# Performance work log

Hardware: AMD Instinct MI355X
Metric: run time of the kernel (lower is better)

## Reference

```python
import jax, jax.numpy as jnp
import numpy as np
import math

B, C, H, W, S = 8, 512, 64, 64, 4


def setup_inputs() -> dict:
    key = jax.random.key(0)
    ks = jax.random.split(key, 7)
    s = 1.0 / math.sqrt(C)  # ~ torch Linear init scale
    x = jax.random.normal(ks[0], (B, C, H, W), jnp.float32)
    Wq = jax.random.uniform(ks[1], (C, C), jnp.float32, -s, s)
    bq = jax.random.uniform(ks[2], (C,), jnp.float32, -s, s)
    Wk = jax.random.uniform(ks[3], (C, C), jnp.float32, -s, s)
    bk = jax.random.uniform(ks[4], (C,), jnp.float32, -s, s)
    Wv = jax.random.uniform(ks[5], (C, C), jnp.float32, -s, s)
    bv = jax.random.uniform(ks[6], (C,), jnp.float32, -s, s)
    return {"x": x, "Wq": Wq, "bq": bq, "Wk": Wk, "bk": bk, "Wv": Wv, "bv": bv}


def reference(x, Wq, bq, Wk, bk, Wv, bv):
    # x: (B, C, H, W). Faithful to the torch module's output, but expressed
    # in the algebraically-equivalent efficient form: the repeat_interleaved
    # attention matrix A is block-constant, so out = repeat(A_m @ Vsum).
    b, c, h, w = x.shape
    nb = (h // S) * (w // S)  # number of SxS spatial blocks
    hw = h * w
    ss = S * S

    # Block means in unfold order (bh, bw): (B, nb, C)
    x_avg = x.reshape(b, c, h // S, S, w // S, S).mean(axis=(3, 5))
    x_avg = x_avg.reshape(b, c, nb).transpose(0, 2, 1)

    Q = x_avg @ Wq.T + bq  # (B, nb, C)
    K = x_avg @ Wk.T + bk  # (B, nb, C)
    A = jax.nn.softmax(jnp.einsum('bnc,bmc->bnm', Q, K) / jnp.sqrt(jnp.float32(c)), axis=-1)

    # V over flat row-major pixels: (B, HW, C)
    x_flat = x.reshape(b, c, hw).transpose(0, 2, 1)
    V = x_flat @ Wv.T + bv

    # repeat_interleave on dim=2 means column group j of A sums V rows
    # [j*ss, (j+1)*ss) in FLAT pixel order (not spatial blocks) - faithful.
    Vsum = V.reshape(b, hw // ss, ss, c).sum(axis=2)  # (B, nb, C)
    out_small = jnp.einsum('bnm,bmc->bnc', A, Vsum)   # (B, nb, C)
    # repeat_interleave on dim=1: each block row broadcast to ss flat pixels
    out_flat = jnp.repeat(out_small, ss, axis=1)      # (B, HW, C)
    return out_flat.transpose(0, 2, 1).reshape(b, c, h, w)
```

## Files before the change

kernel.cpp:

```cpp
#include <hip/hip_runtime.h>

typedef __attribute__((ext_vector_type(8))) short short8;
typedef __attribute__((ext_vector_type(4))) float f32x4;

__device__ __forceinline__ unsigned short f2bf(float f) {
    union { float f; unsigned int i; } v; v.f = f;
    unsigned int x = v.i;
    return (unsigned short)((x + 0x7FFFu + ((x >> 16) & 1u)) >> 16);
}
__device__ __forceinline__ f32x4 mfma16(short8 a, short8 b, f32x4 c) {
    return __builtin_amdgcn_mfma_f32_16x16x32_bf16(a, b, c, 0, 0, 0);
}

__global__ void prep_kernel(const float* __restrict__ x,
                            const float* __restrict__ Wq,
                            const float* __restrict__ Wk,
                            const float* __restrict__ Wv,
                            unsigned short* __restrict__ xavg,
                            unsigned short* __restrict__ xsum,
                            unsigned short* __restrict__ Wb)
{
    const int blk = blockIdx.x;
    const int t = threadIdx.x;
    if (blk >= 4096) {
        const int f = (blk - 4096) * 512 + t;
        const int m = f >> 16;
        const int o = f & 65535;
        const float4* s4 = (const float4*)((m == 0) ? Wq : (m == 1) ? Wk : Wv);
        float4 a = s4[o];
        float4 b = s4[o + 256];
        ushort4* d4 = (ushort4*)(Wb + (size_t)m * 262144);
        d4[o]       = make_ushort4(f2bf(a.x), f2bf(a.y), f2bf(a.z), f2bf(a.w));
        d4[o + 256] = make_ushort4(f2bf(b.x), f2bf(b.y), f2bf(b.z), f2bf(b.w));
        return;
    }
    const int b = blk >> 9;
    const int c = blk & 511;

    const float4* x4 = (const float4*)(x + (size_t)blk * 4096);
    float4 f0 = x4[t], f1 = x4[t + 256], f2 = x4[t + 512], f3 = x4[t + 768];

    __shared__ float part2[1024];
    part2[t]       = f0.x + f0.y + f0.z + f0.w;
    part2[t + 256] = f1.x + f1.y + f1.z + f1.w;
    part2[t + 512] = f2.x + f2.y + f2.z + f2.w;
    part2[t + 768] = f3.x + f3.y + f3.z + f3.w;
    __syncthreads();

    {
        const int base = 16 * (t >> 2) + 4 * (t & 3);
        float4 q = *(const float4*)&part2[base];
        xsum[((size_t)b * 256 + t) * 512 + c] = f2bf(q.x + q.y + q.z + q.w);
    }
    {
        const int bh = t >> 4, bw = t & 15;
        float m = (part2[(bh * 4 + 0) * 16 + bw] + part2[(bh * 4 + 1) * 16 + bw] +
                   part2[(bh * 4 + 2) * 16 + bw] + part2[(bh * 4 + 3) * 16 + bw]) * 0.0625f;
        xavg[((size_t)b * 256 + t) * 512 + c] = f2bf(m);
    }
}

__global__ void __launch_bounds__(256, 3)
proj_gemm(const unsigned short* __restrict__ xavg,
          const unsigned short* __restrict__ xsum,
          const unsigned short* __restrict__ Wb,
          const float* __restrict__ bq,
          const float* __restrict__ bk,
          const float* __restrict__ bv,
          unsigned short* __restrict__ QK,
          unsigned short* __restrict__ VsT)
{
    const int blk = blockIdx.x;
    const int lane = threadIdx.x & 63, quad = lane >> 4, r16 = lane & 15;
    const int w = threadIdx.x >> 6;

    if (blk < 512) {
        const int wave = blk * 4 + w;
        const int mt = wave >> 5;
        const int nt = wave & 31;
        const unsigned short* xp0 = xavg + (size_t)(mt * 32 + r16) * 512 + quad * 8;
        const unsigned short* xp1 = xp0 + 16 * 512;
        const unsigned short* wp0 = Wb + (size_t)(nt * 32 + r16) * 512 + quad * 8;
        const unsigned short* wp1 = wp0 + 16 * 512;

        f32x4 a00 = {0,0,0,0}, a01 = a00, a10 = a00, a11 = a00;
#pragma unroll 4
        for (int k = 0; k < 512; k += 32) {
            short8 qa0 = *(const short8*)(xp0 + k);
            short8 qa1 = *(const short8*)(xp1 + k);
            short8 b0 = *(const short8*)(wp0 + k);
            short8 b1 = *(const short8*)(wp1 + k);
            a00 = mfma16(qa0, b0, a00); a01 = mfma16(qa0, b1, a01);
            a10 = mfma16(qa1, b0, a10); a11 = mfma16(qa1, b1, a11);
        }
        const int row0 = mt * 32 + quad * 4;
        f32x4 accs0[2] = {a00, a01};
        f32x4 accs1[2] = {a10, a11};
#pragma unroll
        for (int j = 0; j < 2; ++j) {
            const int c = nt * 32 + j * 16 + r16;
            const float bias = (c < 512) ? bq[c] : bk[c - 512];
#pragma unroll
            for (int r = 0; r < 4; ++r) {
                QK[(size_t)(row0 + r) * 1024 + c]      = f2bf(accs0[j][r] + bias);
                QK[(size_t)(row0 + 16 + r) * 1024 + c] = f2bf(accs1[j][r] + bias);
            }
        }
    } else {
        const int vblk = blk - 512;
        const int b = vblk >> 5;
        const int wib = (vblk & 31) * 4 + w;
        const int mt2 = wib >> 4;
        const int nt = wib & 15;
        const unsigned short* xp0 = xsum + (size_t)b * 131072 + (size_t)(mt2 * 32 + r16) * 512 + quad * 8;
        const unsigned short* xp1 = xp0 + 16 * 512;
        const unsigned short* wp0 = Wb + 524288 + (size_t)(nt * 32 + r16) * 512 + quad * 8;
        const unsigned short* wp1 = wp0 + 16 * 512;

        f32x4 a00 = {0,0,0,0}, a01 = a00, a10 = a00, a11 = a00;
#pragma unroll 4
        for (int k = 0; k < 512; k += 32) {
            short8 qa0 = *(const short8*)(xp0 + k);
            short8 qa1 = *(const short8*)(xp1 + k);
            short8 b0 = *(const short8*)(wp0 + k);
            short8 b1 = *(const short8*)(wp1 + k);
            a00 = mfma16(qa0, b0, a00); a01 = mfma16(qa0, b1, a01);
            a10 = mfma16(qa1, b0, a10); a11 = mfma16(qa1, b1, a11);
        }
        unsigned short* vb = VsT + (size_t)b * 131072;
        const int m0 = mt2 * 32 + quad * 4;
        f32x4 accs0[2] = {a00, a01};
        f32x4 accs1[2] = {a10, a11};
#pragma unroll
        for (int j = 0; j < 2; ++j) {
            const int c = nt * 32 + j * 16 + r16;
            const float bias = 16.f * bv[c];
#pragma unroll
            for (int r = 0; r < 4; ++r) {
                vb[(size_t)c * 256 + m0 + r]      = f2bf(accs0[j][r] + bias);
                vb[(size_t)c * 256 + m0 + 16 + r] = f2bf(accs1[j][r] + bias);
            }
        }
    }
}

__global__ void __launch_bounds__(256, 2)
score_av(const unsigned short* __restrict__ QK,
         const unsigned short* __restrict__ VsT,
         float* __restrict__ out)
{
    __shared__ union {
        float S[16][257];
        float osT[256][17];
    } u;
    __shared__ __align__(16) unsigned short Abf[16][264];

    const int b = blockIdx.y;
    const int strip = blockIdx.x >> 1;
    const int chalf = blockIdx.x & 1;
    const int w = threadIdx.x >> 6, lane = threadIdx.x & 63;
    const int quad = lane >> 4, r16 = lane & 15;

    {
        const unsigned short* qp = QK + (size_t)(b * 256 + strip * 16 + r16) * 1024 + quad * 8;
        const unsigned short* kp0 = QK + (size_t)(b * 256 + w * 64 + r16) * 1024 + 512 + quad * 8;
        const unsigned short* kp1 = kp0 + 16 * 1024;
        const unsigned short* kp2 = kp0 + 32 * 1024;
        const unsigned short* kp3 = kp0 + 48 * 1024;

        f32x4 a0 = {0,0,0,0}, a1 = a0, a2 = a0, a3 = a0;
#pragma unroll 4
        for (int k = 0; k < 512; k += 32) {
            short8 qa = *(const short8*)(qp + k);
            short8 b0 = *(const short8*)(kp0 + k);
            short8 b1 = *(const short8*)(kp1 + k);
            short8 b2 = *(const short8*)(kp2 + k);
            short8 b3 = *(const short8*)(kp3 + k);
            a0 = mfma16(qa, b0, a0); a1 = mfma16(qa, b1, a1);
            a2 = mfma16(qa, b2, a2); a3 = mfma16(qa, b3, a3);
        }
        f32x4 accs[4] = {a0, a1, a2, a3};
#pragma unroll
        for (int j = 0; j < 4; ++j) {
            const int col = w * 64 + j * 16 + r16;
#pragma unroll
            for (int r = 0; r < 4; ++r)
                u.S[quad * 4 + r][col] = accs[j][r];
        }
    }
    __syncthreads();

    {
        const int t = threadIdx.x;
        const int r = t >> 4, idx = t & 15;
        float v[16];
        float mx = -3.4e38f;
#pragma unroll
        for (int j = 0; j < 16; ++j) {
            v[j] = u.S[r][idx * 16 + j] * 0.044194173824159216f;
            mx = fmaxf(mx, v[j]);
        }
        mx = fmaxf(mx, __shfl_xor(mx, 1));
        mx = fmaxf(mx, __shfl_xor(mx, 2));
        mx = fmaxf(mx, __shfl_xor(mx, 4));
        mx = fmaxf(mx, __shfl_xor(mx, 8));
        float sum = 0.f;
#pragma unroll
        for (int j = 0; j < 16; ++j) { v[j] = __expf(v[j] - mx); sum += v[j]; }
        sum += __shfl_xor(sum, 1);
        sum += __shfl_xor(sum, 2);
        sum += __shfl_xor(sum, 4);
        sum += __shfl_xor(sum, 8);
        const float inv = 1.f / sum;
        unsigned short* ap = &Abf[r][idx * 16];
#pragma unroll
        for (int j = 0; j < 16; j += 4)
            *(ushort4*)(ap + j) = make_ushort4(f2bf(v[j] * inv), f2bf(v[j + 1] * inv),
                                               f2bf(v[j + 2] * inv), f2bf(v[j + 3] * inv));
    }
    __syncthreads();

    {
        f32x4 acc0 = {0,0,0,0}, acc1 = acc0, acc2 = acc0, acc3 = acc0;
        const unsigned short* vbase = VsT + (size_t)b * 131072 +
                                      (size_t)(chalf * 256 + w * 64 + r16) * 256 + quad * 8;
        const unsigned short* vp0 = vbase;
        const unsigned short* vp1 = vbase + 16 * 256;
        const unsigned short* vp2 = vbase + 32 * 256;
        const unsigned short* vp3 = vbase + 48 * 256;
#pragma unroll
        for (int kk = 0; kk < 256; kk += 32) {
            short8 a = *(const short8*)(&Abf[r16][kk + quad * 8]);
            short8 b0 = *(const short8*)(vp0 + kk);
            short8 b1 = *(const short8*)(vp1 + kk);
            short8 b2 = *(const short8*)(vp2 + kk);
            short8 b3 = *(const short8*)(vp3 + kk);
            acc0 = mfma16(a, b0, acc0); acc1 = mfma16(a, b1, acc1);
            acc2 = mfma16(a, b2, acc2); acc3 = mfma16(a, b3, acc3);
        }
        __syncthreads();
        f32x4 accs[4] = {acc0, acc1, acc2, acc3};
#pragma unroll
        for (int i = 0; i < 4; ++i) {
            const int cl = w * 64 + i * 16 + r16;
#pragma unroll
            for (int r = 0; r < 4; ++r)
                u.osT[cl][quad * 4 + r] = accs[i][r];
        }
    }
    __syncthreads();

    {
        const int j = threadIdx.x & 63;
        float* obase = out + (size_t)(b * 512 + chalf * 256) * 4096 + strip * 256 + j * 4;
#pragma unroll
        for (int it = 0; it < 64; ++it) {
            const int ch = it * 4 + w;
            const float v = u.osT[ch][j >> 2];
            *(float4*)(obase + (size_t)ch * 4096) = make_float4(v, v, v, v);
        }
    }
}

extern "C" void kernel_launch(void* const* d_in, const int* in_sizes, int n_in,
                              void* d_out, int out_size, void* d_ws, size_t ws_size,
                              hipStream_t stream) {
    const float* x  = (const float*)d_in[0];
    const float* Wq = (const float*)d_in[1];
    const float* bq = (const float*)d_in[2];
    const float* Wk = (const float*)d_in[3];
    const float* bk = (const float*)d_in[4];
    const float* Wv = (const float*)d_in[5];
    const float* bv = (const float*)d_in[6];
    float* out = (float*)d_out;

    unsigned short* Wb   = (unsigned short*)d_ws;
    unsigned short* xavg = Wb + 786432;
    unsigned short* xsum = xavg + 1048576;
    unsigned short* QK   = xsum + 1048576;
    unsigned short* VsT  = QK + 2097152;

    prep_kernel<<<4480, 256, 0, stream>>>(x, Wq, Wk, Wv, xavg, xsum, Wb);
    proj_gemm<<<768, 256, 0, stream>>>(xavg, xsum, Wb, bq, bk, bv, QK, VsT);
    score_av<<<dim3(32, 8), 256, 0, stream>>>(QK, VsT, out);
}
```

Before: 172.5 us.

## Coalesce prep-kernel transposed writes by processing 16-channel groups per block

Each prep block now handles 16 channels over half the spatial plane instead of one full channel plane. Block sums and means are staged transposed in shared memory so xsum/xavg rows are written as 16-byte vectors rather than scattered 2-byte stores with a 1 KB stride. This removes uncoalesced global writes but adds more syncthreads, a serial loop over channel groups, and fewer blocks (512 instead of 4096) to hide load latency.

```diff
diff --git a/kernel.cpp b/kernel.cpp
--- a/kernel.cpp
+++ b/kernel.cpp
@@ -12,18 +12,19 @@
     return __builtin_amdgcn_mfma_f32_16x16x32_bf16(a, b, c, 0, 0, 0);
 }
 
-__global__ void prep_kernel(const float* __restrict__ x,
-                            const float* __restrict__ Wq,
-                            const float* __restrict__ Wk,
-                            const float* __restrict__ Wv,
-                            unsigned short* __restrict__ xavg,
-                            unsigned short* __restrict__ xsum,
-                            unsigned short* __restrict__ Wb)
+__global__ void __launch_bounds__(256, 4)
+prep_kernel(const float* __restrict__ x,
+            const float* __restrict__ Wq,
+            const float* __restrict__ Wk,
+            const float* __restrict__ Wv,
+            unsigned short* __restrict__ xavg,
+            unsigned short* __restrict__ xsum,
+            unsigned short* __restrict__ Wb)
 {
     const int blk = blockIdx.x;
     const int t = threadIdx.x;
-    if (blk >= 4096) {
-        const int f = (blk - 4096) * 512 + t;
+    if (blk >= 512) {
+        const int f = (blk - 512) * 512 + t;
         const int m = f >> 16;
         const int o = f & 65535;
         const float4* s4 = (const float4*)((m == 0) ? Wq : (m == 1) ? Wk : Wv);
@@ -34,29 +35,71 @@
         d4[o + 256] = make_ushort4(f2bf(b.x), f2bf(b.y), f2bf(b.z), f2bf(b.w));
         return;
     }
-    const int b = blk >> 9;
-    const int c = blk & 511;
-
-    const float4* x4 = (const float4*)(x + (size_t)blk * 4096);
-    float4 f0 = x4[t], f1 = x4[t + 256], f2 = x4[t + 512], f3 = x4[t + 768];
-
-    __shared__ float part2[1024];
-    part2[t]       = f0.x + f0.y + f0.z + f0.w;
-    part2[t + 256] = f1.x + f1.y + f1.z + f1.w;
-    part2[t + 512] = f2.x + f2.y + f2.z + f2.w;
-    part2[t + 768] = f3.x + f3.y + f3.z + f3.w;
-    __syncthreads();
-
-    {
-        const int base = 16 * (t >> 2) + 4 * (t & 3);
-        float4 q = *(const float4*)&part2[base];
-        xsum[((size_t)b * 256 + t) * 512 + c] = f2bf(q.x + q.y + q.z + q.w);
-    }
-    {
-        const int bh = t >> 4, bw = t & 15;
-        float m = (part2[(bh * 4 + 0) * 16 + bw] + part2[(bh * 4 + 1) * 16 + bw] +
-                   part2[(bh * 4 + 2) * 16 + bw] + part2[(bh * 4 + 3) * 16 + bw]) * 0.0625f;
-        xavg[((size_t)b * 256 + t) * 512 + c] = f2bf(m);
+
+    const int b    = blk >> 6;
+    const int rem  = blk & 63;
+    const int cg   = rem >> 1;
+    const int half = rem & 1;
+    const int c0   = cg * 16;
+
+    __shared__ float part[4][512];
+    __shared__ unsigned short xsT[16][128];
+    __shared__ unsigned short xaT[16][128];
+
+    for (int cg4 = 0; cg4 < 4; ++cg4) {
+        float4 a0, a1, b0, b1, c0v, c1, d0, d1;
+        {
+            const float* base = x + ((size_t)(b * 512 + c0 + cg4 * 4) * 4096) + half * 2048;
+            const float4* p0 = (const float4*)(base);
+            const float4* p1 = (const float4*)(base + 4096);
+            const float4* p2 = (const float4*)(base + 8192);
+            const float4* p3 = (const float4*)(base + 12288);
+            a0 = p0[t]; a1 = p0[t + 256];
+            b0 = p1[t]; b1 = p1[t + 256];
+            c0v = p2[t]; c1 = p2[t + 256];
+            d0 = p3[t]; d1 = p3[t + 256];
+        }
+        part[0][t]       = a0.x + a0.y + a0.z + a0.w;
+        part[0][t + 256] = a1.x + a1.y + a1.z + a1.w;
+        part[1][t]       = b0.x + b0.y + b0.z + b0.w;
+        part[1][t + 256] = b1.x + b1.y + b1.z + b1.w;
+        part[2][t]       = c0v.x + c0v.y + c0v.z + c0v.w;
+        part[2][t + 256] = c1.x + c1.y + c1.z + c1.w;
+        part[3][t]       = d0.x + d0.y + d0.z + d0.w;
+        part[3][t + 256] = d1.x + d1.y + d1.z + d1.w;
+        __syncthreads();
+
+        if (t < 128) {
+            const int g = t;
+#pragma unroll
+            for (int ci = 0; ci < 4; ++ci) {
+                float4 q = *(const float4*)&part[ci][4 * g];
+                xsT[cg4 * 4 + ci][g] = f2bf(q.x + q.y + q.z + q.w);
+            }
+        } else {
+            const int n = t - 128;
+            const int bh = n >> 4, bw = n & 15;
+#pragma unroll
+            for (int ci = 0; ci < 4; ++ci) {
+                float m = (part[ci][(bh * 4 + 0) * 16 + bw] + part[ci][(bh * 4 + 1) * 16 + bw] +
+                           part[ci][(bh * 4 + 2) * 16 + bw] + part[ci][(bh * 4 + 3) * 16 + bw]) * 0.0625f;
+                xaT[cg4 * 4 + ci][n] = f2bf(m);
+            }
+        }
+        __syncthreads();
+    }
+
+    {
+        const int g = t >> 1, chunk = t & 1;
+        const size_t rowbase = ((size_t)(b * 256) + half * 128 + g) * 512 + c0 + chunk * 8;
+        short8 vs, va;
+#pragma unroll
+        for (int j = 0; j < 8; ++j) {
+            vs[j] = (short)xsT[chunk * 8 + j][g];
+            va[j] = (short)xaT[chunk * 8 + j][g];
+        }
+        *(short8*)(xsum + rowbase) = vs;
+        *(short8*)(xavg + rowbase) = va;
     }
 }
 
@@ -280,7 +323,7 @@
     unsigned short* QK   = xsum + 1048576;
     unsigned short* VsT  = QK + 2097152;
 
-    prep_kernel<<<4480, 256, 0, stream>>>(x, Wq, Wk, Wv, xavg, xsum, Wb);
+    prep_kernel<<<896, 256, 0, stream>>>(x, Wq, Wk, Wv, xavg, xsum, Wb);
     proj_gemm<<<768, 256, 0, stream>>>(xavg, xsum, Wb, bq, bk, bv, QK, VsT);
     score_av<<<dim3(32, 8), 256, 0, stream>>>(QK, VsT, out);
 }
```

Measured after the change: 164.3 us, median of 2. 1.05x faster.
